# Kernel tuning notes

Hardware: AMD Instinct MI355X
Metric: run time of the kernel (lower is better)

The kernel has to match this reference:

```python
import jax, jax.numpy as jnp
import numpy as np

COST_CLASS = 1.0
COST_MASK = 1.0
COST_DICE = 1.0


def setup_inputs() -> dict:
    key = jax.random.key(0)
    k1, k2, k3, k4 = jax.random.split(key, 4)
    B, Q, T, H, W, C = 4, 100, 20, 128, 128, 80
    out_probs = jax.random.normal(k1, (B, Q, C), dtype=jnp.float32)
    out_masks = jax.random.uniform(k2, (B, Q, H, W), dtype=jnp.float32)
    target_masks = jax.random.uniform(k3, (B, T, H, W), dtype=jnp.float32)
    target_labels = jax.random.randint(k4, (B, T), 0, C, dtype=jnp.int64)
    return {"out_probs": out_probs, "out_masks": out_masks,
            "target_masks": target_masks, "target_labels": target_labels}


def reference(out_probs, out_masks, target_masks, target_labels):
    # out_probs: [B,Q,C]; out_masks: [B,Q,H,W]; target_masks: [B,T,H,W]; target_labels: [B,T]
    B, Q = out_probs.shape[:2]
    T = target_labels.shape[1]

    # Classification cost: -softmax(out_probs)[b, q, target_labels[b, t]] -> [B,Q,T]
    prob = jax.nn.softmax(out_probs, axis=-1)
    idx = jnp.broadcast_to(target_labels[:, None, :], (B, Q, T))
    cost_class = -jnp.take_along_axis(prob, idx, axis=2)

    out_flat = out_masks.reshape(B, Q, -1)      # [B,Q,HW]
    tgt_flat = target_masks.reshape(B, T, -1)   # [B,T,HW]

    # Pairwise L1 cost over pixels: [B,Q,T]
    cost_mask = jnp.abs(out_flat[:, :, None, :] - tgt_flat[:, None, :, :]).sum(-1)

    # Pairwise dice cost: numerator via batched matmul, sums broadcast.
    inter = jnp.einsum('bqn,btn->bqt', out_flat, tgt_flat)
    denom = out_flat.sum(-1)[:, :, None] + tgt_flat.sum(-1)[:, None, :]
    cost_dice = 1.0 - (2.0 * inter + 1.0) / (denom + 1.0)

    C_mat = COST_MASK * cost_mask + COST_CLASS * cost_class + COST_DICE * cost_dice
    return C_mat  # [B,Q,T] cost matrix (Hungarian assignment runs on CPU outside)
```

## Files before the change

kernel.cpp:

```cpp
#include <hip/hip_runtime.h>
#include <hip/hip_bf16.h>
#include <math.h>

#define B_ 4
#define Q_ 100
#define T_ 20
#define C_ 80
#define HW_ 16384
#define HW4_ (HW_ / 4)

#define S_ 8
#define QG_ 4
#define NQG_ (Q_ / QG_)
#define TW_ 5
#define GR_ 2048
#define SGR_ (GR_ / S_)
#define NIT_ (SGR_ / 64)
#define RT_ (B_ * Q_ + B_ * T_)

#define H16_ELEMS ((size_t)RT_ * HW_)
#define RS_F (H16_ELEMS / 2)
#define WL_F (RS_F + 512)
#define WI_F (WL_F + (size_t)B_ * Q_ * T_ * S_ * 4)

typedef float f32x4 __attribute__((ext_vector_type(4)));
typedef unsigned u32x2 __attribute__((ext_vector_type(2)));
typedef unsigned u32x4 __attribute__((ext_vector_type(4)));
typedef _Float16 half2_t __attribute__((ext_vector_type(2)));

__device__ __forceinline__ half2_t h2cast(unsigned u) {
    half2_t r; __builtin_memcpy(&r, &u, 4); return r;
}
__device__ __forceinline__ unsigned u32cast(half2_t v) {
    unsigned u; __builtin_memcpy(&u, &v, 4); return u;
}
__device__ __forceinline__ half2_t habs2(half2_t v) {
    return h2cast(u32cast(v) & 0x7FFF7FFFu);
}
__device__ __forceinline__ unsigned pkrtz_u32(float x, float y) {
    const auto a = __builtin_amdgcn_cvt_pkrtz(x, y);
    unsigned u; __builtin_memcpy(&u, &a, 4); return u;
}
__device__ __forceinline__ u32x4 ldnt4(const u32x4* p) {
    return __builtin_nontemporal_load(p);
}

__device__ __forceinline__ float wred4(float v) {
    v += __shfl_down(v, 32);
    v += __shfl_down(v, 16);
    v += __shfl_down(v, 8);
    v += __shfl_down(v, 4);
    return v;
}

__global__ __launch_bounds__(256) void convert_kernel(const float* __restrict__ outm,
                                                      const float* __restrict__ tgtm,
                                                      _Float16* __restrict__ h16,
                                                      float* __restrict__ fws) {
    const int row = blockIdx.x;
    const float* src = (row < B_ * Q_) ? outm + (size_t)row * HW_
                                       : tgtm + (size_t)(row - B_ * Q_) * HW_;
    const f32x4* s4 = (const f32x4*)src;
    u32x2* d2 = (u32x2*)(h16 + (size_t)row * HW_);

    float sum = 0.f;
    for (int k = threadIdx.x; k < HW4_; k += 256) {
        const f32x4 v = s4[k];
        sum += (v.x + v.y) + (v.z + v.w);
        u32x2 u;
        u.x = pkrtz_u32(v.x, v.y);
        u.y = pkrtz_u32(v.z, v.w);
        d2[k] = u;
    }
    sum += __shfl_down(sum, 32); sum += __shfl_down(sum, 16);
    sum += __shfl_down(sum, 8);  sum += __shfl_down(sum, 4);
    sum += __shfl_down(sum, 2);  sum += __shfl_down(sum, 1);
    __shared__ float red[4];
    if ((threadIdx.x & 63) == 0) red[threadIdx.x >> 6] = sum;
    __syncthreads();
    if (threadIdx.x == 0) fws[RS_F + row] = red[0] + red[1] + red[2] + red[3];
}

__device__ __forceinline__ void cell(u32x4 o, u32x4 g, float& L, float& I) {
    const half2_t o0 = h2cast(o.x), o1 = h2cast(o.y), o2 = h2cast(o.z), o3 = h2cast(o.w);
    const half2_t q0 = h2cast(g.x), q1 = h2cast(g.y), q2 = h2cast(g.z), q3 = h2cast(g.w);
    I = __builtin_amdgcn_fdot2(o0, q0, I, false);
    I = __builtin_amdgcn_fdot2(o1, q1, I, false);
    I = __builtin_amdgcn_fdot2(o2, q2, I, false);
    I = __builtin_amdgcn_fdot2(o3, q3, I, false);
    const half2_t d0 = habs2(o0 - q0), d1 = habs2(o1 - q1);
    const half2_t d2 = habs2(o2 - q2), d3 = habs2(o3 - q3);
    const half2_t s = (d0 + d1) + (d2 + d3);
    half2_t ones; ones.x = (_Float16)1.f; ones.y = (_Float16)1.f;
    L = __builtin_amdgcn_fdot2(s, ones, L, false);
}

__global__ __launch_bounds__(256) void partial_kernel(const _Float16* __restrict__ h16,
                                                      float* __restrict__ fws) {
    const int r = blockIdx.x & 7;
    const int m = blockIdx.x >> 3;
    const int b = r >> 1;
    const int l = m * 2 + (r & 1);
    const int qg = l >> 3;
    const int seg = l & (S_ - 1);

    const int lane = threadIdx.x & 63;
    const int ts   = threadIdx.x >> 6;
    const int t0   = ts * TW_;

    const u32x4* ob = (const u32x4*)(h16 + (size_t)(b * Q_ + qg * QG_) * HW_) + seg * SGR_ + lane;
    const u32x4* gb = (const u32x4*)(h16 + (size_t)(B_ * Q_ + b * T_) * HW_) + seg * SGR_ + lane;

    float accL[QG_][TW_], accI[QG_][TW_];
#pragma unroll
    for (int qi = 0; qi < QG_; ++qi)
#pragma unroll
        for (int tj = 0; tj < TW_; ++tj) { accL[qi][tj] = 0.f; accI[qi][tj] = 0.f; }

#pragma unroll
    for (int it = 0; it < NIT_; ++it) {
        const int ofs = it * 64;
        u32x4 o[QG_];
#pragma unroll
        for (int qi = 0; qi < QG_; ++qi) o[qi] = ldnt4(ob + (size_t)qi * GR_ + ofs);
#pragma unroll
        for (int tj = 0; tj < TW_; ++tj) {
            const u32x4 g = gb[(size_t)(t0 + tj) * GR_ + ofs];
#pragma unroll
            for (int qi = 0; qi < QG_; ++qi)
                cell(o[qi], g, accL[qi][tj], accI[qi][tj]);
        }
    }

    float* WL = fws + WL_F;
    float* WI = fws + WI_F;
#pragma unroll
    for (int qi = 0; qi < QG_; ++qi) {
        const int bq = b * Q_ + qg * QG_ + qi;
#pragma unroll
        for (int tj = 0; tj < TW_; ++tj) {
            const float vL = wred4(accL[qi][tj]);
            const float vI = wred4(accI[qi][tj]);
            if (lane < 4) {
                const size_t idx = ((size_t)bq * T_ + t0 + tj) * (S_ * 4) + seg * 4 + lane;
                WL[idx] = vL;
                WI[idx] = vI;
            }
        }
    }
}

__global__ __launch_bounds__(64) void finalize_kernel(const float* __restrict__ probs,
                                                      const int*   __restrict__ labels,
                                                      const float* __restrict__ fws,
                                                      float* __restrict__ out) {
    const int bq = blockIdx.x;
    const int b = bq / Q_;

    __shared__ float s_logit[C_];
    for (int c = threadIdx.x; c < C_; c += 64)
        s_logit[c] = probs[(size_t)bq * C_ + c];
    __syncthreads();

    const int t = threadIdx.x;
    if (t < T_) {
        const float4* WL4 = (const float4*)(fws + WL_F) + ((size_t)bq * T_ + t) * S_;
        const float4* WI4 = (const float4*)(fws + WI_F) + ((size_t)bq * T_ + t) * S_;
        float L = 0.f, I = 0.f;
#pragma unroll
        for (int s = 0; s < S_; ++s) {
            const float4 a = WL4[s];
            const float4 v = WI4[s];
            L += (a.x + a.y) + (a.z + a.w);
            I += (v.x + v.y) + (v.z + v.w);
        }
        const float osum = fws[RS_F + bq];
        const float tsum = fws[RS_F + B_ * Q_ + b * T_ + t];

        float mx = -INFINITY;
#pragma unroll
        for (int c = 0; c < C_; ++c) mx = fmaxf(mx, s_logit[c]);
        float sum = 0.f;
#pragma unroll
        for (int c = 0; c < C_; ++c) sum += __expf(s_logit[c] - mx);
        const int lab = labels[(size_t)b * T_ + t];
        const float p = __expf(s_logit[lab] - mx) / sum;

        const float denom = osum + tsum;
        const float dice = 1.f - (2.f * I + 1.f) / (denom + 1.f);

        out[(size_t)bq * T_ + t] = L - p + dice;
    }
}

extern "C" void kernel_launch(void* const* d_in, const int* in_sizes, int n_in,
                              void* d_out, int out_size, void* d_ws, size_t ws_size,
                              hipStream_t stream) {
    const float* out_probs     = (const float*)d_in[0];
    const float* out_masks     = (const float*)d_in[1];
    const float* target_masks  = (const float*)d_in[2];
    const int*   target_labels = (const int*)d_in[3];
    float* out = (float*)d_out;

    _Float16* h16 = (_Float16*)d_ws;
    float* fws    = (float*)d_ws;

    convert_kernel<<<RT_, 256, 0, stream>>>(out_masks, target_masks, h16, fws);
    partial_kernel<<<B_ * NQG_ * S_, 256, 0, stream>>>(h16, fws);
    finalize_kernel<<<B_ * Q_, 64, 0, stream>>>(out_probs, target_labels, fws, out);
}
```

Measured before the change: 37.26 us.

## Fuse output-mask fp16 conversion and row sums into the pairwise partial kernel

Only target masks are pre-converted to fp16. Output masks are read as fp32 directly in the partial kernel, packed to fp16 in registers, and their row sums are accumulated there. Target row sums are computed by the first q-pair blocks, and the finalize kernel reduces the per-segment sums. This removes the fp16 write and re-read of all output masks, but halves the query grouping, so target tiles are reloaded more often and the pair kernel carries more register work.

```diff
diff --git a/kernel.cpp b/kernel.cpp
--- a/kernel.cpp
+++ b/kernel.cpp
@@ -10,18 +10,18 @@
 #define HW4_ (HW_ / 4)
 
 #define S_ 8
-#define QG_ 4
-#define NQG_ (Q_ / QG_)
+#define QP_ (Q_ / 2)
+#define SEGF4_ (HW4_ / S_)
+#define SEGG_ (HW_ / 8 / S_)
+#define NIT_ 4
 #define TW_ 5
-#define GR_ 2048
-#define SGR_ (GR_ / S_)
-#define NIT_ (SGR_ / 64)
-#define RT_ (B_ * Q_ + B_ * T_)
-
-#define H16_ELEMS ((size_t)RT_ * HW_)
-#define RS_F (H16_ELEMS / 2)
-#define WL_F (RS_F + 512)
+
+#define G16_ELEMS ((size_t)B_ * T_ * HW_)
+#define FB_ (G16_ELEMS / 2)
+#define WL_F FB_
 #define WI_F (WL_F + (size_t)B_ * Q_ * T_ * S_ * 4)
+#define OS_F (WI_F + (size_t)B_ * Q_ * T_ * S_ * 4)
+#define GS_F (OS_F + (size_t)B_ * Q_ * S_ * 4)
 
 typedef float f32x4 __attribute__((ext_vector_type(4)));
 typedef unsigned u32x2 __attribute__((ext_vector_type(2)));
@@ -40,9 +40,6 @@
 __device__ __forceinline__ unsigned pkrtz_u32(float x, float y) {
     const auto a = __builtin_amdgcn_cvt_pkrtz(x, y);
     unsigned u; __builtin_memcpy(&u, &a, 4); return u;
-}
-__device__ __forceinline__ u32x4 ldnt4(const u32x4* p) {
-    return __builtin_nontemporal_load(p);
 }
 
 __device__ __forceinline__ float wred4(float v) {
@@ -53,32 +50,20 @@
     return v;
 }
 
-__global__ __launch_bounds__(256) void convert_kernel(const float* __restrict__ outm,
-                                                      const float* __restrict__ tgtm,
-                                                      _Float16* __restrict__ h16,
-                                                      float* __restrict__ fws) {
-    const int row = blockIdx.x;
-    const float* src = (row < B_ * Q_) ? outm + (size_t)row * HW_
-                                       : tgtm + (size_t)(row - B_ * Q_) * HW_;
-    const f32x4* s4 = (const f32x4*)src;
-    u32x2* d2 = (u32x2*)(h16 + (size_t)row * HW_);
-
-    float sum = 0.f;
-    for (int k = threadIdx.x; k < HW4_; k += 256) {
-        const f32x4 v = s4[k];
-        sum += (v.x + v.y) + (v.z + v.w);
+__global__ __launch_bounds__(256) void gconv_kernel(const float* __restrict__ tgtm,
+                                                    _Float16* __restrict__ g16) {
+    const int row  = blockIdx.x >> 2;
+    const int part = blockIdx.x & 3;
+    const f32x4* s4 = (const f32x4*)(tgtm + (size_t)row * HW_);
+    u32x2* d2 = (u32x2*)(g16 + (size_t)row * HW_);
+    const int base = part * (HW4_ / 4);
+    for (int k = threadIdx.x; k < HW4_ / 4; k += 256) {
+        const f32x4 v = __builtin_nontemporal_load(s4 + base + k);
         u32x2 u;
         u.x = pkrtz_u32(v.x, v.y);
         u.y = pkrtz_u32(v.z, v.w);
-        d2[k] = u;
-    }
-    sum += __shfl_down(sum, 32); sum += __shfl_down(sum, 16);
-    sum += __shfl_down(sum, 8);  sum += __shfl_down(sum, 4);
-    sum += __shfl_down(sum, 2);  sum += __shfl_down(sum, 1);
-    __shared__ float red[4];
-    if ((threadIdx.x & 63) == 0) red[threadIdx.x >> 6] = sum;
-    __syncthreads();
-    if (threadIdx.x == 0) fws[RS_F + row] = red[0] + red[1] + red[2] + red[3];
+        __builtin_nontemporal_store(u, d2 + base + k);
+    }
 }
 
 __device__ __forceinline__ void cell(u32x4 o, u32x4 g, float& L, float& I) {
@@ -95,48 +80,68 @@
     L = __builtin_amdgcn_fdot2(s, ones, L, false);
 }
 
-__global__ __launch_bounds__(256) void partial_kernel(const _Float16* __restrict__ h16,
-                                                      float* __restrict__ fws) {
-    const int r = blockIdx.x & 7;
-    const int m = blockIdx.x >> 3;
-    const int b = r >> 1;
-    const int l = m * 2 + (r & 1);
-    const int qg = l >> 3;
-    const int seg = l & (S_ - 1);
-
-    const int lane = threadIdx.x & 63;
-    const int ts   = threadIdx.x >> 6;
-    const int t0   = ts * TW_;
-
-    const u32x4* ob = (const u32x4*)(h16 + (size_t)(b * Q_ + qg * QG_) * HW_) + seg * SGR_ + lane;
-    const u32x4* gb = (const u32x4*)(h16 + (size_t)(B_ * Q_ + b * T_) * HW_) + seg * SGR_ + lane;
-
-    float accL[QG_][TW_], accI[QG_][TW_];
-#pragma unroll
-    for (int qi = 0; qi < QG_; ++qi)
+template <bool WITH_G>
+__device__ __forceinline__ void partial_body(const f32x4* __restrict__ o0p,
+                                             const f32x4* __restrict__ o1p,
+                                             const u32x4* __restrict__ gb,
+                                             float* __restrict__ fws,
+                                             int qpair, int b, int seg,
+                                             int lane, int ts) {
+    const int t0 = ts * TW_;
+
+    float accL[2][TW_], accI[2][TW_], os[2], gs[TW_];
+#pragma unroll
+    for (int qi = 0; qi < 2; ++qi) {
+        os[qi] = 0.f;
 #pragma unroll
         for (int tj = 0; tj < TW_; ++tj) { accL[qi][tj] = 0.f; accI[qi][tj] = 0.f; }
+    }
+#pragma unroll
+    for (int tj = 0; tj < TW_; ++tj) gs[tj] = 0.f;
 
 #pragma unroll
     for (int it = 0; it < NIT_; ++it) {
-        const int ofs = it * 64;
-        u32x4 o[QG_];
-#pragma unroll
-        for (int qi = 0; qi < QG_; ++qi) o[qi] = ldnt4(ob + (size_t)qi * GR_ + ofs);
+        u32x4 g[TW_];
+#pragma unroll
+        for (int tj = 0; tj < TW_; ++tj)
+            g[tj] = gb[(size_t)(t0 + tj) * (HW_ / 8) + it * 64 + lane];
+        const int fo = it * 128 + 2 * lane;
+        const f32x4 a0 = o0p[fo], a1 = o0p[fo + 1];
+        const f32x4 b0 = o1p[fo], b1 = o1p[fo + 1];
+
+        if (ts == 0) {
+            os[0] += ((a0.x + a0.y) + (a0.z + a0.w)) + ((a1.x + a1.y) + (a1.z + a1.w));
+            os[1] += ((b0.x + b0.y) + (b0.z + b0.w)) + ((b1.x + b1.y) + (b1.z + b1.w));
+        }
+        if (WITH_G) {
+            half2_t ones; ones.x = (_Float16)1.f; ones.y = (_Float16)1.f;
+#pragma unroll
+            for (int tj = 0; tj < TW_; ++tj) {
+                gs[tj] = __builtin_amdgcn_fdot2(h2cast(g[tj].x), ones, gs[tj], false);
+                gs[tj] = __builtin_amdgcn_fdot2(h2cast(g[tj].y), ones, gs[tj], false);
+                gs[tj] = __builtin_amdgcn_fdot2(h2cast(g[tj].z), ones, gs[tj], false);
+                gs[tj] = __builtin_amdgcn_fdot2(h2cast(g[tj].w), ones, gs[tj], false);
+            }
+        }
+        u32x4 oq0, oq1;
+        oq0.x = pkrtz_u32(a0.x, a0.y); oq0.y = pkrtz_u32(a0.z, a0.w);
+        oq0.z = pkrtz_u32(a1.x, a1.y); oq0.w = pkrtz_u32(a1.z, a1.w);
+        oq1.x = pkrtz_u32(b0.x, b0.y); oq1.y = pkrtz_u32(b0.z, b0.w);
+        oq1.z = pkrtz_u32(b1.x, b1.y); oq1.w = pkrtz_u32(b1.z, b1.w);
 #pragma unroll
         for (int tj = 0; tj < TW_; ++tj) {
-            const u32x4 g = gb[(size_t)(t0 + tj) * GR_ + ofs];
-#pragma unroll
-            for (int qi = 0; qi < QG_; ++qi)
-                cell(o[qi], g, accL[qi][tj], accI[qi][tj]);
+            cell(oq0, g[tj], accL[0][tj], accI[0][tj]);
+            cell(oq1, g[tj], accL[1][tj], accI[1][tj]);
         }
     }
 
     float* WL = fws + WL_F;
     float* WI = fws + WI_F;
-#pragma unroll
-    for (int qi = 0; qi < QG_; ++qi) {
-        const int bq = b * Q_ + qg * QG_ + qi;
+    float* OS = fws + OS_F;
+    float* GS = fws + GS_F;
+#pragma unroll
+    for (int qi = 0; qi < 2; ++qi) {
+        const int bq = b * Q_ + qpair * 2 + qi;
 #pragma unroll
         for (int tj = 0; tj < TW_; ++tj) {
             const float vL = wred4(accL[qi][tj]);
@@ -147,7 +152,39 @@
                 WI[idx] = vI;
             }
         }
-    }
+        if (ts == 0) {
+            const float vo = wred4(os[qi]);
+            if (lane < 4) OS[(size_t)bq * (S_ * 4) + seg * 4 + lane] = vo;
+        }
+    }
+    if (WITH_G) {
+#pragma unroll
+        for (int tj = 0; tj < TW_; ++tj) {
+            const float vg = wred4(gs[tj]);
+            if (lane < 4) GS[(size_t)(b * T_ + t0 + tj) * (S_ * 4) + seg * 4 + lane] = vg;
+        }
+    }
+}
+
+__global__ __launch_bounds__(256) void partial_kernel(const float* __restrict__ outm,
+                                                      const _Float16* __restrict__ g16,
+                                                      float* __restrict__ fws) {
+    const int r = blockIdx.x & 7;
+    const int m = blockIdx.x >> 3;
+    const int b = r >> 1;
+    const int l = m * 2 + (r & 1);
+    const int qp = l >> 3;
+    const int seg = l & (S_ - 1);
+
+    const int lane = threadIdx.x & 63;
+    const int ts   = threadIdx.x >> 6;
+
+    const f32x4* o0p = (const f32x4*)(outm + ((size_t)b * Q_ + qp * 2) * HW_) + seg * SEGF4_;
+    const f32x4* o1p = o0p + HW4_;
+    const u32x4* gb  = (const u32x4*)(g16 + (size_t)b * T_ * HW_) + seg * SEGG_;
+
+    if (qp == 0) partial_body<true>(o0p, o1p, gb, fws, qp, b, seg, lane, ts);
+    else         partial_body<false>(o0p, o1p, gb, fws, qp, b, seg, lane, ts);
 }
 
 __global__ __launch_bounds__(64) void finalize_kernel(const float* __restrict__ probs,
@@ -166,17 +203,20 @@
     if (t < T_) {
         const float4* WL4 = (const float4*)(fws + WL_F) + ((size_t)bq * T_ + t) * S_;
         const float4* WI4 = (const float4*)(fws + WI_F) + ((size_t)bq * T_ + t) * S_;
-        float L = 0.f, I = 0.f;
+        const float4* OS4 = (const float4*)(fws + OS_F) + (size_t)bq * S_;
+        const float4* GS4 = (const float4*)(fws + GS_F) + ((size_t)b * T_ + t) * S_;
+        float L = 0.f, I = 0.f, osum = 0.f, tsum = 0.f;
 #pragma unroll
         for (int s = 0; s < S_; ++s) {
             const float4 a = WL4[s];
             const float4 v = WI4[s];
-            L += (a.x + a.y) + (a.z + a.w);
-            I += (v.x + v.y) + (v.z + v.w);
-        }
-        const float osum = fws[RS_F + bq];
-        const float tsum = fws[RS_F + B_ * Q_ + b * T_ + t];
-
+            const float4 c = OS4[s];
+            const float4 d = GS4[s];
+            L    += (a.x + a.y) + (a.z + a.w);
+            I    += (v.x + v.y) + (v.z + v.w);
+            osum += (c.x + c.y) + (c.z + c.w);
+            tsum += (d.x + d.y) + (d.z + d.w);
+        }
         float mx = -INFINITY;
 #pragma unroll
         for (int c = 0; c < C_; ++c) mx = fmaxf(mx, s_logit[c]);
@@ -202,10 +242,10 @@
     const int*   target_labels = (const int*)d_in[3];
     float* out = (float*)d_out;
 
-    _Float16* h16 = (_Float16*)d_ws;
+    _Float16* g16 = (_Float16*)d_ws;
     float* fws    = (float*)d_ws;
 
-    convert_kernel<<<RT_, 256, 0, stream>>>(out_masks, target_masks, h16, fws);
-    partial_kernel<<<B_ * NQG_ * S_, 256, 0, stream>>>(h16, fws);
+    gconv_kernel<<<B_ * T_ * 4, 256, 0, stream>>>(target_masks, g16);
+    partial_kernel<<<B_ * QP_ * S_, 256, 0, stream>>>(out_masks, g16, fws);
     finalize_kernel<<<B_ * Q_, 64, 0, stream>>>(out_probs, target_labels, fws, out);
 }
```

Result: no change. 37.56 us (+0.8%).
